# Kernel tuning notes

Measured on AMD Instinct MI355X. Metric: run time of the kernel, lower is better.

The kernel has to match this reference:

```python
import jax, jax.numpy as jnp
import numpy as np

N = 8192
D_IN = 128
D_OUT = 64
NEG_SLOPE = 0.2
MASK_VAL = -9e15


def setup_inputs() -> dict:
    key = jax.random.key(0)
    k_in, k_adj, k_w, k_a = jax.random.split(key, 4)
    inp = jax.random.normal(k_in, (1, N, D_IN), dtype=jnp.float32)
    adj = jax.random.uniform(k_adj, (N, N), dtype=jnp.float32)
    # xavier_uniform with gain=1.414
    gain = 1.414
    bw = gain * np.sqrt(6.0 / (D_IN + D_OUT))
    w = jax.random.uniform(k_w, (D_IN, D_OUT), dtype=jnp.float32, minval=-bw, maxval=bw)
    ba = gain * np.sqrt(6.0 / (2 * D_OUT + 1))
    a = jax.random.uniform(k_a, (2 * D_OUT, 1), dtype=jnp.float32, minval=-ba, maxval=ba)
    a_coeff = jnp.ones((1,), dtype=jnp.float32)
    b_coeff = jnp.ones((1,), dtype=jnp.float32)
    return {"input": inp, "adj": adj, "w": w, "a": a, "a_coeff": a_coeff, "b_coeff": b_coeff}


def reference(input, adj, w, a, a_coeff, b_coeff):
    h = input[0] @ w                      # [N, D_OUT]
    # e[i,j] = [h_i, h_j] . a  ==  (h @ a1)_i + (h @ a2)_j  (fused, no N^2*2D concat)
    a1 = a[:D_OUT, 0]
    a2 = a[D_OUT:, 0]
    e = (h @ a1)[:, None] + (h @ a2)[None, :]             # [N, N]
    adj_t = a_coeff[0] * adj + b_coeff[0]
    lrelu = jnp.where(adj_t >= 0, adj_t, NEG_SLOPE * adj_t)
    e_t = lrelu * e
    attn = jnp.where(adj > 0, e_t, jnp.float32(MASK_VAL))
    attn = jax.nn.softmax(attn, axis=1)                    # masked row softmax
    h_prime = attn @ h                                     # [N, D_OUT]
    return jax.nn.elu(h_prime)                             # concat=True -> elu
```

## Files before the change

kernel.cpp:

```cpp
#include <hip/hip_runtime.h>

#define NN 8192
#define DIN 128
#define DOUT 64

typedef __attribute__((ext_vector_type(8))) short short8;
typedef __attribute__((ext_vector_type(4))) float f32x4;

static __device__ __forceinline__ unsigned short f2bf(float x) {
  unsigned u = __builtin_bit_cast(unsigned, x);
  u = (u + 0x7FFFu + ((u >> 16) & 1u)) >> 16;
  return (unsigned short)u;
}

__global__ __launch_bounds__(256) void k_h(
    const float* __restrict__ x, const float* __restrict__ wmat,
    const float* __restrict__ avec, float* __restrict__ f,
    float* __restrict__ g, unsigned short* __restrict__ hbf) {
  const int t = threadIdx.x;
  const int lane = t & 63;
  const int row = blockIdx.x * 4 + (t >> 6);
  const float* xr = x + (size_t)row * DIN;
  float acc = 0.f;
#pragma unroll 8
  for (int k = 0; k < DIN; ++k) acc = fmaf(xr[k], wmat[k * DOUT + lane], acc);

  float fa = acc * avec[lane];
  float ga = acc * avec[DOUT + lane];
#pragma unroll
  for (int off = 32; off; off >>= 1) {
    fa += __shfl_xor(fa, off);
    ga += __shfl_xor(ga, off);
  }
  if (lane == 0) { f[row] = fa; g[row] = ga; }

  const int jt  = row >> 5;
  const int grp = (row >> 3) & 3;
  const int e   = row & 7;
  const int ns  = lane >> 4;
  const int l15 = lane & 15;
  hbf[((size_t)(jt * 4 + ns) * 64 + grp * 16 + l15) * 8 + e] = f2bf(acc);
}

__global__ __launch_bounds__(256, 4) void k_main(
    const float* __restrict__ adj, const float* __restrict__ f,
    const float* __restrict__ g, const unsigned short* __restrict__ hbf,
    const float* __restrict__ acp, const float* __restrict__ bcp,
    float* __restrict__ pacc, float* __restrict__ pms) {
  const int t = threadIdx.x;
  const int wv = t >> 6, lane = t & 63;
  const int r = lane & 15, grp = lane >> 4;
  const int stripe = blockIdx.x >> 1;
  const int half = blockIdx.x & 1;
  const int i0 = stripe * 16;
  const float ac = acp[0], bc = bcp[0];
  const float fr = f[i0 + r];
  const float L2E = 1.4426950408889634f;
  const float MASKV = -9.0e15f;

  float m = MASKV, s = 0.f;
  f32x4 acc0 = {0.f, 0.f, 0.f, 0.f};
  f32x4 acc1 = acc0, acc2 = acc0, acc3 = acc0;

  const float* arow = adj + (size_t)(i0 + r) * NN;
  const int jtEnd = half * 128 + 128;

  int jt0 = half * 128 + wv;
  float4 A0 = *reinterpret_cast<const float4*>(arow + jt0 * 32 + grp * 8);
  float4 A1 = *reinterpret_cast<const float4*>(arow + jt0 * 32 + grp * 8 + 4);

  for (int jt = jt0; jt < jtEnd; jt += 4) {
    const int jn = (jt + 4 < jtEnd) ? jt + 4 : jt;
    const float4 nA0 = *reinterpret_cast<const float4*>(arow + jn * 32 + grp * 8);
    const float4 nA1 = *reinterpret_cast<const float4*>(arow + jn * 32 + grp * 8 + 4);

    const int jb = jt * 32 + grp * 8;
    const float4 G0 = *reinterpret_cast<const float4*>(g + jb);
    const float4 G1 = *reinterpret_cast<const float4*>(g + jb + 4);
    const short8* bp = reinterpret_cast<const short8*>(hbf) + (size_t)jt * 256 + lane;
    const short8 B0 = bp[0], B1 = bp[64], B2 = bp[128], B3 = bp[192];

    const float av[8] = {A0.x, A0.y, A0.z, A0.w, A1.x, A1.y, A1.z, A1.w};
    const float gv[8] = {G0.x, G0.y, G0.z, G0.w, G1.x, G1.y, G1.z, G1.w};
    float sc[8];
    float tmax = MASKV;
#pragma unroll
    for (int e = 0; e < 8; ++e) {
      const float adjv = av[e];
      const float tl = fmaf(ac, adjv, bc);
      const float lr = fmaxf(tl, 0.2f * tl);
      float sv = lr * (fr + gv[e]);
      sv = adjv > 0.f ? sv : MASKV;
      sc[e] = sv;
      tmax = fmaxf(tmax, sv);
    }
    tmax = fmaxf(tmax, __shfl_xor(tmax, 16));
    tmax = fmaxf(tmax, __shfl_xor(tmax, 32));

    if (__any(tmax > m + 8.f)) {
      const float mn = fmaxf(m, tmax);
      const float scale = exp2f((m - mn) * L2E);
      s *= scale;
      const float s0 = __shfl(scale, grp * 4 + 0);
      const float s1 = __shfl(scale, grp * 4 + 1);
      const float s2 = __shfl(scale, grp * 4 + 2);
      const float s3 = __shfl(scale, grp * 4 + 3);
      const f32x4 sv4 = {s0, s1, s2, s3};
      acc0 *= sv4; acc1 *= sv4; acc2 *= sv4; acc3 *= sv4;
      m = mn;
    }

    const float mL = m * L2E;
    short8 afrag;
    float ps = 0.f;
#pragma unroll
    for (int e = 0; e < 8; ++e) {
      const float p = exp2f(fmaf(sc[e], L2E, -mL));
      ps += p;
      afrag[e] = (short)f2bf(p);
    }
    s += ps;

    acc0 = __builtin_amdgcn_mfma_f32_16x16x32_bf16(afrag, B0, acc0, 0, 0, 0);
    acc1 = __builtin_amdgcn_mfma_f32_16x16x32_bf16(afrag, B1, acc1, 0, 0, 0);
    acc2 = __builtin_amdgcn_mfma_f32_16x16x32_bf16(afrag, B2, acc2, 0, 0, 0);
    acc3 = __builtin_amdgcn_mfma_f32_16x16x32_bf16(afrag, B3, acc3, 0, 0, 0);

    A0 = nA0; A1 = nA1;
  }

  s += __shfl_xor(s, 16);
  s += __shfl_xor(s, 32);

  __shared__ float sm[4][16];
  __shared__ float ssum[4][16];
  __shared__ float sacc[4][16][65];
  if (grp == 0) { sm[wv][r] = m; ssum[wv][r] = s; }
#pragma unroll
  for (int reg = 0; reg < 4; ++reg) {
    sacc[wv][grp * 4 + reg][ 0 + r] = acc0[reg];
    sacc[wv][grp * 4 + reg][16 + r] = acc1[reg];
    sacc[wv][grp * 4 + reg][32 + r] = acc2[reg];
    sacc[wv][grp * 4 + reg][48 + r] = acc3[reg];
  }
  __syncthreads();

  const int c = t & 63;
  float* paccB = pacc + (size_t)blockIdx.x * 16 * 64;
  float* pmsB  = pms  + (size_t)blockIdx.x * 32;
#pragma unroll
  for (int rr = 0; rr < 4; ++rr) {
    const int row = (t >> 6) * 4 + rr;
    const float M = fmaxf(fmaxf(sm[0][row], sm[1][row]),
                          fmaxf(sm[2][row], sm[3][row]));
    float S = 0.f, A = 0.f;
#pragma unroll
    for (int k = 0; k < 4; ++k) {
      const float e = exp2f((sm[k][row] - M) * L2E);
      S += ssum[k][row] * e;
      A += sacc[k][row][c] * e;
    }
    paccB[row * 64 + c] = A;
    if (c == 0) { pmsB[row * 2] = M; pmsB[row * 2 + 1] = S; }
  }
}

__global__ __launch_bounds__(256) void k_comb(
    const float* __restrict__ pacc, const float* __restrict__ pms,
    float* __restrict__ out) {
  const int idx = blockIdx.x * 256 + threadIdx.x;
  const int row = idx >> 6, c = idx & 63;
  const int stripe = row >> 4, rin = row & 15;
  const float L2E = 1.4426950408889634f;
  const size_t b0 = (size_t)stripe * 2, b1 = b0 + 1;
  const float m0 = pms[b0 * 32 + rin * 2], s0 = pms[b0 * 32 + rin * 2 + 1];
  const float m1 = pms[b1 * 32 + rin * 2], s1 = pms[b1 * 32 + rin * 2 + 1];
  const float M = fmaxf(m0, m1);
  const float e0 = exp2f((m0 - M) * L2E);
  const float e1 = exp2f((m1 - M) * L2E);
  const float A = pacc[b0 * 1024 + rin * 64 + c] * e0 +
                  pacc[b1 * 1024 + rin * 64 + c] * e1;
  const float S = s0 * e0 + s1 * e1;
  const float v = A / S;
  out[idx] = v > 0.f ? v : expm1f(v);
}

extern "C" void kernel_launch(void* const* d_in, const int* in_sizes, int n_in,
                              void* d_out, int out_size, void* d_ws, size_t ws_size,
                              hipStream_t stream) {
  const float* x    = (const float*)d_in[0];
  const float* adj  = (const float*)d_in[1];
  const float* wmat = (const float*)d_in[2];
  const float* avec = (const float*)d_in[3];
  const float* acp  = (const float*)d_in[4];
  const float* bcp  = (const float*)d_in[5];
  float* out = (float*)d_out;

  float* f = (float*)d_ws;
  float* g = f + NN;
  unsigned short* hbf = (unsigned short*)(g + NN);
  float* pacc = (float*)(hbf + (size_t)NN * DOUT);
  float* pms  = pacc + (size_t)1024 * 16 * 64;

  k_h<<<NN / 4, 256, 0, stream>>>(x, wmat, avec, f, g, hbf);
  k_main<<<NN / 8, 256, 0, stream>>>(adj, f, g, hbf, acp, bcp, pacc, pms);
  k_comb<<<NN * DOUT / 256, 256, 0, stream>>>(pacc, pms, out);
}
```

Before: 97.28 us.

## Stream adjacency tiles into LDS via async global_load_lds double buffering

Replaces the per-lane register prefetch of adjacency values with direct global-to-LDS async loads into a double-buffered 16x256 shared tile. The layout is XOR-swizzled to avoid bank conflicts, and each wave now processes two 32-column subtiles per tile. The goal is to keep more adjacency bytes in flight and hide HBM latency on this bandwidth-bound N^2 read. In exchange it adds a __syncthreads per tile and 32KB of LDS per block, and the LDS is reused for the epilogue. That may reduce occupancy compared with the launch bound of 4 blocks.

```diff
diff --git a/kernel.cpp b/kernel.cpp
--- a/kernel.cpp
+++ b/kernel.cpp
@@ -3,6 +3,8 @@
 #define NN 8192
 #define DIN 128
 #define DOUT 64
+#define TK 256
+#define NTILE 16
 
 typedef __attribute__((ext_vector_type(8))) short short8;
 typedef __attribute__((ext_vector_type(4))) float f32x4;
@@ -11,6 +13,12 @@
   unsigned u = __builtin_bit_cast(unsigned, x);
   u = (u + 0x7FFFu + ((u >> 16) & 1u)) >> 16;
   return (unsigned short)u;
+}
+
+static __device__ __forceinline__ void gload_lds16(const float* src, float* dst) {
+  __builtin_amdgcn_global_load_lds(
+      (const __attribute__((address_space(1))) void*)src,
+      (__attribute__((address_space(3))) void*)dst, 16, 0, 0);
 }
 
 __global__ __launch_bounds__(256) void k_h(
@@ -47,12 +55,14 @@
     const float* __restrict__ g, const unsigned short* __restrict__ hbf,
     const float* __restrict__ acp, const float* __restrict__ bcp,
     float* __restrict__ pacc, float* __restrict__ pms) {
+  __shared__ float smem[2][16][TK];
   const int t = threadIdx.x;
   const int wv = t >> 6, lane = t & 63;
   const int r = lane & 15, grp = lane >> 4;
   const int stripe = blockIdx.x >> 1;
   const int half = blockIdx.x & 1;
   const int i0 = stripe * 16;
+  const int c0 = half * 4096;
   const float ac = acp[0], bc = bcp[0];
   const float fr = f[i0 + r];
   const float L2E = 1.4426950408889634f;
@@ -62,86 +72,115 @@
   f32x4 acc0 = {0.f, 0.f, 0.f, 0.f};
   f32x4 acc1 = acc0, acc2 = acc0, acc3 = acc0;
 
-  const float* arow = adj + (size_t)(i0 + r) * NN;
-  const int jtEnd = half * 128 + 128;
-
-  int jt0 = half * 128 + wv;
-  float4 A0 = *reinterpret_cast<const float4*>(arow + jt0 * 32 + grp * 8);
-  float4 A1 = *reinterpret_cast<const float4*>(arow + jt0 * 32 + grp * 8 + 4);
-
-  for (int jt = jt0; jt < jtEnd; jt += 4) {
-    const int jn = (jt + 4 < jtEnd) ? jt + 4 : jt;
-    const float4 nA0 = *reinterpret_cast<const float4*>(arow + jn * 32 + grp * 8);
-    const float4 nA1 = *reinterpret_cast<const float4*>(arow + jn * 32 + grp * 8 + 4);
-
-    const int jb = jt * 32 + grp * 8;
-    const float4 G0 = *reinterpret_cast<const float4*>(g + jb);
-    const float4 G1 = *reinterpret_cast<const float4*>(g + jb + 4);
-    const short8* bp = reinterpret_cast<const short8*>(hbf) + (size_t)jt * 256 + lane;
-    const short8 B0 = bp[0], B1 = bp[64], B2 = bp[128], B3 = bp[192];
-
-    const float av[8] = {A0.x, A0.y, A0.z, A0.w, A1.x, A1.y, A1.z, A1.w};
-    const float gv[8] = {G0.x, G0.y, G0.z, G0.w, G1.x, G1.y, G1.z, G1.w};
-    float sc[8];
-    float tmax = MASKV;
-#pragma unroll
-    for (int e = 0; e < 8; ++e) {
-      const float adjv = av[e];
-      const float tl = fmaf(ac, adjv, bc);
-      const float lr = fmaxf(tl, 0.2f * tl);
-      float sv = lr * (fr + gv[e]);
-      sv = adjv > 0.f ? sv : MASKV;
-      sc[e] = sv;
-      tmax = fmaxf(tmax, sv);
+#pragma unroll
+  for (int rr = 0; rr < 4; ++rr) {
+    const int sr = wv * 4 + rr;
+    gload_lds16(adj + (size_t)(i0 + sr) * NN + c0 + ((lane ^ sr) << 2),
+                &smem[0][sr][0]);
+  }
+  __syncthreads();
+
+  for (int tile = 0; tile < NTILE; ++tile) {
+    const int cur = tile & 1;
+    const int jta = half * 128 + tile * 8 + wv * 2;
+    const int jtb = jta + 1;
+
+    const int jba = jta * 32 + grp * 8;
+    const int jbb = jtb * 32 + grp * 8;
+    const float4 Ga0 = *(const float4*)(g + jba);
+    const float4 Ga1 = *(const float4*)(g + jba + 4);
+    const float4 Gb0 = *(const float4*)(g + jbb);
+    const float4 Gb1 = *(const float4*)(g + jbb + 4);
+    const short8* bpa = (const short8*)hbf + (size_t)jta * 256 + lane;
+    const short8* bpb = (const short8*)hbf + (size_t)jtb * 256 + lane;
+    const short8 Ba0 = bpa[0], Ba1 = bpa[64], Ba2 = bpa[128], Ba3 = bpa[192];
+    const short8 Bb0 = bpb[0], Bb1 = bpb[64], Bb2 = bpb[128], Bb3 = bpb[192];
+
+    __builtin_amdgcn_sched_barrier(0);
+    if (tile + 1 < NTILE) {
+      const int cc = c0 + (tile + 1) * TK;
+#pragma unroll
+      for (int rr = 0; rr < 4; ++rr) {
+        const int sr = wv * 4 + rr;
+        gload_lds16(adj + (size_t)(i0 + sr) * NN + cc + ((lane ^ sr) << 2),
+                    &smem[cur ^ 1][sr][0]);
+      }
     }
-    tmax = fmaxf(tmax, __shfl_xor(tmax, 16));
-    tmax = fmaxf(tmax, __shfl_xor(tmax, 32));
-
-    if (__any(tmax > m + 8.f)) {
-      const float mn = fmaxf(m, tmax);
-      const float scale = exp2f((m - mn) * L2E);
-      s *= scale;
-      const float s0 = __shfl(scale, grp * 4 + 0);
-      const float s1 = __shfl(scale, grp * 4 + 1);
-      const float s2 = __shfl(scale, grp * 4 + 2);
-      const float s3 = __shfl(scale, grp * 4 + 3);
-      const f32x4 sv4 = {s0, s1, s2, s3};
-      acc0 *= sv4; acc1 *= sv4; acc2 *= sv4; acc3 *= sv4;
-      m = mn;
-    }
-
-    const float mL = m * L2E;
-    short8 afrag;
-    float ps = 0.f;
-#pragma unroll
-    for (int e = 0; e < 8; ++e) {
-      const float p = exp2f(fmaf(sc[e], L2E, -mL));
-      ps += p;
-      afrag[e] = (short)f2bf(p);
-    }
-    s += ps;
-
-    acc0 = __builtin_amdgcn_mfma_f32_16x16x32_bf16(afrag, B0, acc0, 0, 0, 0);
-    acc1 = __builtin_amdgcn_mfma_f32_16x16x32_bf16(afrag, B1, acc1, 0, 0, 0);
-    acc2 = __builtin_amdgcn_mfma_f32_16x16x32_bf16(afrag, B2, acc2, 0, 0, 0);
-    acc3 = __builtin_amdgcn_mfma_f32_16x16x32_bf16(afrag, B3, acc3, 0, 0, 0);
-
-    A0 = nA0; A1 = nA1;
+    __builtin_amdgcn_sched_barrier(0);
+
+    auto subtile = [&](int jl, const float4& G0, const float4& G1,
+                       const short8& B0, const short8& B1,
+                       const short8& B2, const short8& B3) {
+      const int u0 = (jl * 8 + grp * 2);
+      const float4 A0 = *(const float4*)&smem[cur][r][(u0 ^ r) << 2];
+      const float4 A1 = *(const float4*)&smem[cur][r][((u0 + 1) ^ r) << 2];
+      const float av[8] = {A0.x, A0.y, A0.z, A0.w, A1.x, A1.y, A1.z, A1.w};
+      const float gv[8] = {G0.x, G0.y, G0.z, G0.w, G1.x, G1.y, G1.z, G1.w};
+      float sc[8];
+      float tmax = MASKV;
+#pragma unroll
+      for (int e = 0; e < 8; ++e) {
+        const float adjv = av[e];
+        const float tl = fmaf(ac, adjv, bc);
+        const float lr = fmaxf(tl, 0.2f * tl);
+        float sv = lr * (fr + gv[e]);
+        sv = adjv > 0.f ? sv : MASKV;
+        sc[e] = sv;
+        tmax = fmaxf(tmax, sv);
+      }
+      tmax = fmaxf(tmax, __shfl_xor(tmax, 16));
+      tmax = fmaxf(tmax, __shfl_xor(tmax, 32));
+
+      if (__any(tmax > m + 8.f)) {
+        const float mn = fmaxf(m, tmax);
+        const float scale = exp2f((m - mn) * L2E);
+        s *= scale;
+        const float s0 = __shfl(scale, grp * 4 + 0);
+        const float s1 = __shfl(scale, grp * 4 + 1);
+        const float s2 = __shfl(scale, grp * 4 + 2);
+        const float s3 = __shfl(scale, grp * 4 + 3);
+        const f32x4 sv4 = {s0, s1, s2, s3};
+        acc0 *= sv4; acc1 *= sv4; acc2 *= sv4; acc3 *= sv4;
+        m = mn;
+      }
+
+      const float mL = m * L2E;
+      short8 afrag;
+      float ps = 0.f;
+#pragma unroll
+      for (int e = 0; e < 8; ++e) {
+        const float p = exp2f(fmaf(sc[e], L2E, -mL));
+        ps += p;
+        afrag[e] = (short)f2bf(p);
+      }
+      s += ps;
+
+      acc0 = __builtin_amdgcn_mfma_f32_16x16x32_bf16(afrag, B0, acc0, 0, 0, 0);
+      acc1 = __builtin_amdgcn_mfma_f32_16x16x32_bf16(afrag, B1, acc1, 0, 0, 0);
+      acc2 = __builtin_amdgcn_mfma_f32_16x16x32_bf16(afrag, B2, acc2, 0, 0, 0);
+      acc3 = __builtin_amdgcn_mfma_f32_16x16x32_bf16(afrag, B3, acc3, 0, 0, 0);
+    };
+    subtile(wv * 2,     Ga0, Ga1, Ba0, Ba1, Ba2, Ba3);
+    subtile(wv * 2 + 1, Gb0, Gb1, Bb0, Bb1, Bb2, Bb3);
+
+    __syncthreads();
   }
 
   s += __shfl_xor(s, 16);
   s += __shfl_xor(s, 32);
 
-  __shared__ float sm[4][16];
-  __shared__ float ssum[4][16];
-  __shared__ float sacc[4][16][65];
-  if (grp == 0) { sm[wv][r] = m; ssum[wv][r] = s; }
+  float* base = &smem[0][0][0];
+  float* sacc_ = base;
+  float* sm_   = base + 4160;
+  float* ss_   = base + 4224;
+  if (grp == 0) { sm_[wv * 16 + r] = m; ss_[wv * 16 + r] = s; }
 #pragma unroll
   for (int reg = 0; reg < 4; ++reg) {
-    sacc[wv][grp * 4 + reg][ 0 + r] = acc0[reg];
-    sacc[wv][grp * 4 + reg][16 + r] = acc1[reg];
-    sacc[wv][grp * 4 + reg][32 + r] = acc2[reg];
-    sacc[wv][grp * 4 + reg][48 + r] = acc3[reg];
+    const int rowi = grp * 4 + reg;
+    sacc_[(wv * 16 + rowi) * 65 +  0 + r] = acc0[reg];
+    sacc_[(wv * 16 + rowi) * 65 + 16 + r] = acc1[reg];
+    sacc_[(wv * 16 + rowi) * 65 + 32 + r] = acc2[reg];
+    sacc_[(wv * 16 + rowi) * 65 + 48 + r] = acc3[reg];
   }
   __syncthreads();
 
@@ -151,14 +190,14 @@
 #pragma unroll
   for (int rr = 0; rr < 4; ++rr) {
     const int row = (t >> 6) * 4 + rr;
-    const float M = fmaxf(fmaxf(sm[0][row], sm[1][row]),
-                          fmaxf(sm[2][row], sm[3][row]));
+    const float M = fmaxf(fmaxf(sm_[0 * 16 + row], sm_[1 * 16 + row]),
+                          fmaxf(sm_[2 * 16 + row], sm_[3 * 16 + row]));
     float S = 0.f, A = 0.f;
 #pragma unroll
     for (int k = 0; k < 4; ++k) {
-      const float e = exp2f((sm[k][row] - M) * L2E);
-      S += ssum[k][row] * e;
-      A += sacc[k][row][c] * e;
+      const float e = exp2f((sm_[k * 16 + row] - M) * L2E);
+      S += ss_[k * 16 + row] * e;
+      A += sacc_[(k * 16 + row) * 65 + c] * e;
     }
     paccB[row * 64 + c] = A;
     if (c == 0) { pmsB[row * 2] = M; pmsB[row * 2 + 1] = S; }
```

Measured after the change: 95.45 us. Within noise of the previous version (-1.9%).
